# Kernel optimization log

Measured on AMD Instinct MI355X. Metric: run time of the kernel, lower is better.

## Reference

```python
import jax, jax.numpy as jnp
import numpy as np

EPS = 1e-12  # matches torch F.normalize default

def _l2norm(x):
    n = jnp.linalg.norm(x, axis=-1, keepdims=True)
    return x / jnp.maximum(n, EPS)

def setup_inputs() -> dict:
    key = jax.random.key(0)
    k1, k2, k3, k4 = jax.random.split(key, 4)
    return {
        "shape_embedding": jax.random.normal(k1, (4096, 512), dtype=jnp.float32),
        "bank_embedding": jax.random.normal(k2, (100000, 512), dtype=jnp.float32),
        "category_idx": jax.random.randint(k3, (100000,), 0, 9, dtype=jnp.int64),
        "shape_idx": jax.random.randint(k4, (100000,), 0, 10000, dtype=jnp.int64),
    }

def reference(shape_embedding, bank_embedding, category_idx, shape_idx):
    # bank is stored L2-normalized in __init__; query normalized in forward
    q = _l2norm(shape_embedding)          # [N, D]
    b = _l2norm(bank_embedding)           # [M, D]
    sims = jnp.einsum('nd,md->nm', q, b)  # [N, M] cosine similarity
    idx = jnp.argmax(sims, axis=-1)       # [N]
    return (category_idx[idx], shape_idx[idx])
```

## Files before the change

kernel.cpp:

```cpp
#include <hip/hip_runtime.h>
#include <math.h>

#define NQ  4096
#define MB  100000
#define DD  512
#define QT  128
#define BT  128
#define BK  32
#define KIT (DD / BK)
#define NCH ((MB + BT - 1) / BT)
#define NWG (32 * NCH)
#define MARGIN 6e-3f

typedef __attribute__((ext_vector_type(8))) short short8;
typedef __attribute__((ext_vector_type(4))) float f32x4;

__device__ inline unsigned int umax32(unsigned int a, unsigned int b) { return a > b ? a : b; }
__device__ inline unsigned int umin32(unsigned int a, unsigned int b) { return a < b ? a : b; }

__device__ inline unsigned short f2bf(float f) {
  unsigned int u = __float_as_uint(f);
  u += 0x7FFFu + ((u >> 16) & 1u);
  return (unsigned short)(u >> 16);
}

__device__ inline void gload_lds16(const void* g, void* l) {
  __builtin_amdgcn_global_load_lds(
      (const __attribute__((address_space(1))) unsigned int*)g,
      (__attribute__((address_space(3))) unsigned int*)l, 16, 0, 0);
}

__global__ __launch_bounds__(256) void nrm_cast(const float* __restrict__ qin,
                                                const float* __restrict__ bin,
                                                unsigned short* __restrict__ qb,
                                                unsigned short* __restrict__ bb) {
  int wave = threadIdx.x >> 6, lane = threadIdx.x & 63;
  int row = blockIdx.x * 4 + wave;
  const float* src;
  unsigned short* dst;
  if (row < NQ) {
    src = qin + (size_t)row * DD;
    dst = qb + (size_t)row * DD;
  } else {
    int r2 = row - NQ;
    if (r2 >= MB) return;
    src = bin + (size_t)r2 * DD;
    dst = bb + (size_t)r2 * DD;
  }
  const float4* s4 = (const float4*)src;
  float4 x0 = s4[lane * 2], x1 = s4[lane * 2 + 1];
  float ss = x0.x * x0.x + x0.y * x0.y + x0.z * x0.z + x0.w * x0.w +
             x1.x * x1.x + x1.y * x1.y + x1.z * x1.z + x1.w * x1.w;
  #pragma unroll
  for (int m = 1; m < 64; m <<= 1) ss += __shfl_xor(ss, m, 64);
  float r = 1.0f / fmaxf(sqrtf(ss), 1e-12f);
  short8 v;
  v[0] = (short)f2bf(x0.x * r); v[1] = (short)f2bf(x0.y * r);
  v[2] = (short)f2bf(x0.z * r); v[3] = (short)f2bf(x0.w * r);
  v[4] = (short)f2bf(x1.x * r); v[5] = (short)f2bf(x1.y * r);
  v[6] = (short)f2bf(x1.z * r); v[7] = (short)f2bf(x1.w * r);
  *(short8*)(dst + (size_t)lane * 8) = v;
}

__global__ __launch_bounds__(256, 3) void gemm_top2(
    const unsigned short* __restrict__ qb,
    const unsigned short* __restrict__ bb,
    uint2* __restrict__ cand) {
  __shared__ unsigned short sM[2][BT * BK];
  __shared__ unsigned short sN[2][QT * BK];
  __shared__ unsigned int rowwin[QT][2][2];

  int tid = threadIdx.x;
  int wave = tid >> 6, lane = tid & 63;

  int w = blockIdx.x;
  int sw = (w & 7) * (NWG / 8) + (w >> 3);
  int bx = sw & 31;
  int by = sw >> 5;
  int q0 = bx * QT, c0 = by * BT;
  int wm = (wave >> 1) * 64;
  int wn = (wave & 1) * 64;

  f32x4 acc[4][4];
  #pragma unroll
  for (int i = 0; i < 4; ++i)
    #pragma unroll
    for (int j = 0; j < 4; ++j) acc[i][j] = (f32x4){0.f, 0.f, 0.f, 0.f};

  int sr = tid >> 2;
  int slot = tid & 3;
  int swz = (tid >> 4) & 3;
  int ce = (slot ^ swz) * 8;
  int br0 = c0 + sr;       if (br0 >= MB) br0 = MB - 1;
  int br1 = c0 + 64 + sr;  if (br1 >= MB) br1 = MB - 1;

  int rr = lane & 15;
  int ck = lane >> 4;
  int rco = (ck ^ ((rr >> 2) & 3)) * 8;

  const unsigned short* gM0 = bb + (size_t)br0 * DD + ce;
  const unsigned short* gM1 = bb + (size_t)br1 * DD + ce;
  const unsigned short* gN0 = qb + (size_t)(q0 + sr) * DD + ce;
  const unsigned short* gN1 = qb + (size_t)(q0 + 64 + sr) * DD + ce;

  auto STAGE = [&](int kt, int buf) {
    int kk = kt * BK;
    gload_lds16(gM0 + kk, &sM[buf][tid * 8]);
    gload_lds16(gM1 + kk, &sM[buf][2048 + tid * 8]);
    gload_lds16(gN0 + kk, &sN[buf][tid * 8]);
    gload_lds16(gN1 + kk, &sN[buf][2048 + tid * 8]);
  };

  STAGE(0, 0);
  __syncthreads();

  #pragma unroll 2
  for (int kt = 0; kt < KIT; ++kt) {
    int cur = kt & 1;
    if (kt + 1 < KIT) STAGE(kt + 1, cur ^ 1);

    const unsigned short* M0 = sM[cur];
    const unsigned short* N0 = sN[cur];
    short8 af[4], bg[4];
    #pragma unroll
    for (int mi = 0; mi < 4; ++mi)
      af[mi] = *(const short8*)&M0[(wm + mi * 16 + rr) * BK + rco];
    #pragma unroll
    for (int ni = 0; ni < 4; ++ni)
      bg[ni] = *(const short8*)&N0[(wn + ni * 16 + rr) * BK + rco];
    #pragma unroll
    for (int mi = 0; mi < 4; ++mi)
      #pragma unroll
      for (int ni = 0; ni < 4; ++ni)
        acc[mi][ni] = __builtin_amdgcn_mfma_f32_16x16x32_bf16(af[mi], bg[ni],
                                                              acc[mi][ni], 0, 0, 0);
    __syncthreads();
  }

  int g = lane >> 4, cl = lane & 15;
  bool tail = (c0 + BT > MB);
  int nb = 127 - wm - g * 4;
  unsigned int K1[4], K2[4];
  #pragma unroll
  for (int ni = 0; ni < 4; ++ni) { K1[ni] = 0u; K2[ni] = 0u; }

  #pragma unroll
  for (int mi = 0; mi < 4; ++mi) {
    #pragma unroll
    for (int r2 = 0; r2 < 4; ++r2) {
      int rowoff = mi * 16 + r2;
      #pragma unroll
      for (int ni = 0; ni < 4; ++ni) {
        float v = acc[mi][ni][r2];
        unsigned int key = (__float_as_uint(v) & 0xFFFFFF80u) |
                           (unsigned int)(nb - rowoff);
        bool ok = v > 0.0f;
        if (tail) ok = ok && (c0 + wm + g * 4 + rowoff < MB);
        key = ok ? key : 0u;
        unsigned int mx = umax32(K1[ni], key), mn = umin32(K1[ni], key);
        K1[ni] = mx;
        K2[ni] = umax32(K2[ni], mn);
      }
    }
  }

  #pragma unroll
  for (int m = 16; m <= 32; m <<= 1) {
    #pragma unroll
    for (int ni = 0; ni < 4; ++ni) {
      unsigned int o1 = (unsigned int)__shfl_xor((int)K1[ni], m, 64);
      unsigned int o2 = (unsigned int)__shfl_xor((int)K2[ni], m, 64);
      unsigned int mx = umax32(K1[ni], o1), mn = umin32(K1[ni], o1);
      K1[ni] = mx;
      K2[ni] = umax32(mn, umax32(K2[ni], o2));
    }
  }
  if (g == 0) {
    #pragma unroll
    for (int ni = 0; ni < 4; ++ni) {
      int qc = wn + ni * 16 + cl;
      rowwin[qc][wave >> 1][0] = K1[ni];
      rowwin[qc][wave >> 1][1] = K2[ni];
    }
  }
  __syncthreads();

  if (tid < QT) {
    unsigned int a1 = rowwin[tid][0][0], a2 = rowwin[tid][0][1];
    unsigned int b1 = rowwin[tid][1][0], b2 = rowwin[tid][1][1];
    unsigned int k1 = umax32(a1, b1);
    unsigned int k2 = umax32(umin32(a1, b1), umax32(a2, b2));
    cand[(size_t)by * NQ + q0 + tid] = make_uint2(k1, k2);
  }
}

__global__ __launch_bounds__(256) void reduce_refine(
    const float* __restrict__ qraw, const float* __restrict__ braw,
    const int* __restrict__ cat, const int* __restrict__ shp,
    const uint2* __restrict__ cand, int* __restrict__ out) {
  int q = blockIdx.x;
  int tid = threadIdx.x, wave = tid >> 6, lane = tid & 63;
  __shared__ unsigned int wmax[4];
  __shared__ int nsel;
  __shared__ int sel[64];
  __shared__ float rv[64];
  __shared__ int ri[64];
  if (tid == 0) nsel = 0;

  unsigned int mk = 0;
  for (int c = tid; c < NCH; c += 256) mk = umax32(mk, cand[(size_t)c * NQ + q].x);
  #pragma unroll
  for (int m = 1; m < 64; m <<= 1)
    mk = umax32(mk, (unsigned int)__shfl_xor((int)mk, m, 64));
  if (lane == 0) wmax[wave] = mk;
  __syncthreads();
  unsigned int M1 = umax32(umax32(wmax[0], wmax[1]), umax32(wmax[2], wmax[3]));
  float thr = __uint_as_float(M1 & 0xFFFFFF80u) - MARGIN;

  for (int c = tid; c < NCH; c += 256) {
    uint2 e = cand[(size_t)c * NQ + q];
    float f1 = __uint_as_float(e.x & 0xFFFFFF80u);
    float f2 = __uint_as_float(e.y & 0xFFFFFF80u);
    if (f1 >= thr) {
      int p = atomicAdd(&nsel, 1);
      if (p < 64) sel[p] = c * BT + 127 - (int)(e.x & 127u);
    }
    if (f2 >= thr) {
      int p = atomicAdd(&nsel, 1);
      if (p < 64) sel[p] = c * BT + 127 - (int)(e.y & 127u);
    }
  }
  __syncthreads();
  int ns = nsel; if (ns > 64) ns = 64;

  const float4* q4 = (const float4*)(qraw + (size_t)q * DD);
  float4 qa = q4[lane * 2], qv = q4[lane * 2 + 1];
  float qss = qa.x * qa.x + qa.y * qa.y + qa.z * qa.z + qa.w * qa.w +
              qv.x * qv.x + qv.y * qv.y + qv.z * qv.z + qv.w * qv.w;
  #pragma unroll
  for (int m = 1; m < 64; m <<= 1) qss += __shfl_xor(qss, m, 64);
  float qn = fmaxf(sqrtf(qss), 1e-12f);

  for (int ci = wave; ci < ns; ci += 4) {
    int bi = sel[ci];
    const float4* b4 = (const float4*)(braw + (size_t)bi * DD);
    float4 ba = b4[lane * 2], bv = b4[lane * 2 + 1];
    float dot = qa.x * ba.x + qa.y * ba.y + qa.z * ba.z + qa.w * ba.w +
                qv.x * bv.x + qv.y * bv.y + qv.z * bv.z + qv.w * bv.w;
    float bss = ba.x * ba.x + ba.y * ba.y + ba.z * ba.z + ba.w * ba.w +
                bv.x * bv.x + bv.y * bv.y + bv.z * bv.z + bv.w * bv.w;
    #pragma unroll
    for (int m = 1; m < 64; m <<= 1) {
      dot += __shfl_xor(dot, m, 64);
      bss += __shfl_xor(bss, m, 64);
    }
    if (lane == 0) {
      float bn = fmaxf(sqrtf(bss), 1e-12f);
      rv[ci] = dot / (qn * bn);
      ri[ci] = bi;
    }
  }
  __syncthreads();

  if (tid == 0) {
    float bvv = rv[0]; int bidx = ri[0];
    for (int i = 1; i < ns; ++i)
      if (rv[i] > bvv || (rv[i] == bvv && ri[i] < bidx)) { bvv = rv[i]; bidx = ri[i]; }
    out[q] = cat[bidx];
    out[NQ + q] = shp[bidx];
  }
}

extern "C" void kernel_launch(void* const* d_in, const int* in_sizes, int n_in,
                              void* d_out, int out_size, void* d_ws, size_t ws_size,
                              hipStream_t stream) {
  const float* qin = (const float*)d_in[0];
  const float* bin = (const float*)d_in[1];
  const int* cat = (const int*)d_in[2];
  const int* shp = (const int*)d_in[3];
  int* out = (int*)d_out;

  char* ws = (char*)d_ws;
  unsigned short* qb = (unsigned short*)ws;
  unsigned short* bb = (unsigned short*)(ws + (size_t)NQ * DD * 2);
  uint2* cand = (uint2*)(ws + (size_t)NQ * DD * 2 + (size_t)MB * DD * 2);

  nrm_cast<<<(NQ + MB) / 4, 256, 0, stream>>>(qin, bin, qb, bb);
  gemm_top2<<<NWG, 256, 0, stream>>>(qb, bb, cand);
  reduce_refine<<<NQ, 256, 0, stream>>>(qin, bin, cat, shp, cand, out);
}
```

Before: 868.3 us.

## Batch 64 queries per block in refine and overlap LDS staging with MFMA

The refine kernel now gives each block 64 queries, with one lane per query, so each wave reads contiguous cand entries across queries instead of strided single-query reads. Selected candidates go into a shared work queue that all waves then process. Separately, the GEMM main loop swaps __syncthreads for a partial vmcnt wait plus raw barriers, so the next tile's global-to-LDS load overlaps the current tile's MFMAs. Risks: candidates per query are capped at 16 (was 64), the query norm is recomputed for each candidate, and a single thread serially builds the queue.

```diff
diff --git a/kernel.cpp b/kernel.cpp
--- a/kernel.cpp
+++ b/kernel.cpp
@@ -11,6 +11,7 @@
 #define NCH ((MB + BT - 1) / BT)
 #define NWG (32 * NCH)
 #define MARGIN 6e-3f
+#define RQ  64
 
 typedef __attribute__((ext_vector_type(8))) short short8;
 typedef __attribute__((ext_vector_type(4))) float f32x4;
@@ -111,16 +112,9 @@
     gload_lds16(gN1 + kk, &sN[buf][2048 + tid * 8]);
   };
 
-  STAGE(0, 0);
-  __syncthreads();
-
-  #pragma unroll 2
-  for (int kt = 0; kt < KIT; ++kt) {
-    int cur = kt & 1;
-    if (kt + 1 < KIT) STAGE(kt + 1, cur ^ 1);
-
-    const unsigned short* M0 = sM[cur];
-    const unsigned short* N0 = sN[cur];
+  auto COMPUTE = [&](int buf) {
+    const unsigned short* M0 = sM[buf];
+    const unsigned short* N0 = sN[buf];
     short8 af[4], bg[4];
     #pragma unroll
     for (int mi = 0; mi < 4; ++mi)
@@ -134,8 +128,22 @@
       for (int ni = 0; ni < 4; ++ni)
         acc[mi][ni] = __builtin_amdgcn_mfma_f32_16x16x32_bf16(af[mi], bg[ni],
                                                               acc[mi][ni], 0, 0, 0);
-    __syncthreads();
-  }
+  };
+
+  STAGE(0, 0);
+  for (int kt = 0; kt < KIT - 1; ++kt) {
+    STAGE(kt + 1, (kt & 1) ^ 1);
+    asm volatile("s_waitcnt vmcnt(4)" ::: "memory");
+    __builtin_amdgcn_s_barrier();
+    __builtin_amdgcn_sched_barrier(0);
+    COMPUTE(kt & 1);
+    __builtin_amdgcn_sched_barrier(0);
+    __builtin_amdgcn_s_barrier();
+  }
+  asm volatile("s_waitcnt vmcnt(0)" ::: "memory");
+  __builtin_amdgcn_s_barrier();
+  __builtin_amdgcn_sched_barrier(0);
+  COMPUTE((KIT - 1) & 1);
 
   int g = lane >> 4, cl = lane & 15;
   bool tail = (c0 + BT > MB);
@@ -198,74 +206,89 @@
     const float* __restrict__ qraw, const float* __restrict__ braw,
     const int* __restrict__ cat, const int* __restrict__ shp,
     const uint2* __restrict__ cand, int* __restrict__ out) {
-  int q = blockIdx.x;
   int tid = threadIdx.x, wave = tid >> 6, lane = tid & 63;
-  __shared__ unsigned int wmax[4];
-  __shared__ int nsel;
-  __shared__ int sel[64];
-  __shared__ float rv[64];
-  __shared__ int ri[64];
-  if (tid == 0) nsel = 0;
+  int q0 = blockIdx.x * RQ;
+  int q = q0 + lane;
+
+  __shared__ unsigned int wm[4][RQ];
+  __shared__ int cnt[RQ];
+  __shared__ int sel[RQ][16];
+  __shared__ float rvv[RQ][16];
+  __shared__ unsigned short queue[RQ * 16];
+  __shared__ int qn;
 
   unsigned int mk = 0;
-  for (int c = tid; c < NCH; c += 256) mk = umax32(mk, cand[(size_t)c * NQ + q].x);
-  #pragma unroll
-  for (int m = 1; m < 64; m <<= 1)
-    mk = umax32(mk, (unsigned int)__shfl_xor((int)mk, m, 64));
-  if (lane == 0) wmax[wave] = mk;
-  __syncthreads();
-  unsigned int M1 = umax32(umax32(wmax[0], wmax[1]), umax32(wmax[2], wmax[3]));
+  for (int c = wave; c < NCH; c += 4)
+    mk = umax32(mk, cand[(size_t)c * NQ + q].x);
+  wm[wave][lane] = mk;
+  if (wave == 0) cnt[lane] = 0;
+  __syncthreads();
+  unsigned int M1 = umax32(umax32(wm[0][lane], wm[1][lane]),
+                           umax32(wm[2][lane], wm[3][lane]));
   float thr = __uint_as_float(M1 & 0xFFFFFF80u) - MARGIN;
 
-  for (int c = tid; c < NCH; c += 256) {
+  for (int c = wave; c < NCH; c += 4) {
     uint2 e = cand[(size_t)c * NQ + q];
     float f1 = __uint_as_float(e.x & 0xFFFFFF80u);
     float f2 = __uint_as_float(e.y & 0xFFFFFF80u);
     if (f1 >= thr) {
-      int p = atomicAdd(&nsel, 1);
-      if (p < 64) sel[p] = c * BT + 127 - (int)(e.x & 127u);
+      int p = atomicAdd(&cnt[lane], 1);
+      if (p < 16) sel[lane][p] = c * BT + 127 - (int)(e.x & 127u);
     }
     if (f2 >= thr) {
-      int p = atomicAdd(&nsel, 1);
-      if (p < 64) sel[p] = c * BT + 127 - (int)(e.y & 127u);
-    }
-  }
-  __syncthreads();
-  int ns = nsel; if (ns > 64) ns = 64;
-
-  const float4* q4 = (const float4*)(qraw + (size_t)q * DD);
-  float4 qa = q4[lane * 2], qv = q4[lane * 2 + 1];
-  float qss = qa.x * qa.x + qa.y * qa.y + qa.z * qa.z + qa.w * qa.w +
-              qv.x * qv.x + qv.y * qv.y + qv.z * qv.z + qv.w * qv.w;
-  #pragma unroll
-  for (int m = 1; m < 64; m <<= 1) qss += __shfl_xor(qss, m, 64);
-  float qn = fmaxf(sqrtf(qss), 1e-12f);
-
-  for (int ci = wave; ci < ns; ci += 4) {
-    int bi = sel[ci];
+      int p = atomicAdd(&cnt[lane], 1);
+      if (p < 16) sel[lane][p] = c * BT + 127 - (int)(e.y & 127u);
+    }
+  }
+  __syncthreads();
+
+  if (tid == 0) {
+    int t = 0;
+    for (int i = 0; i < RQ; ++i) {
+      int n = cnt[i] < 16 ? cnt[i] : 16;
+      for (int s = 0; s < n; ++s) queue[t++] = (unsigned short)((i << 4) | s);
+    }
+    qn = t;
+  }
+  __syncthreads();
+
+  int total = qn;
+  for (int e = wave; e < total; e += 4) {
+    int ql = queue[e] >> 4, sl = queue[e] & 15;
+    int bi = sel[ql][sl];
+    const float4* q4 = (const float4*)(qraw + (size_t)(q0 + ql) * DD);
     const float4* b4 = (const float4*)(braw + (size_t)bi * DD);
+    float4 qa = q4[lane * 2], qv = q4[lane * 2 + 1];
     float4 ba = b4[lane * 2], bv = b4[lane * 2 + 1];
     float dot = qa.x * ba.x + qa.y * ba.y + qa.z * ba.z + qa.w * ba.w +
                 qv.x * bv.x + qv.y * bv.y + qv.z * bv.z + qv.w * bv.w;
+    float qss = qa.x * qa.x + qa.y * qa.y + qa.z * qa.z + qa.w * qa.w +
+                qv.x * qv.x + qv.y * qv.y + qv.z * qv.z + qv.w * qv.w;
     float bss = ba.x * ba.x + ba.y * ba.y + ba.z * ba.z + ba.w * ba.w +
                 bv.x * bv.x + bv.y * bv.y + bv.z * bv.z + bv.w * bv.w;
     #pragma unroll
     for (int m = 1; m < 64; m <<= 1) {
       dot += __shfl_xor(dot, m, 64);
+      qss += __shfl_xor(qss, m, 64);
       bss += __shfl_xor(bss, m, 64);
     }
     if (lane == 0) {
-      float bn = fmaxf(sqrtf(bss), 1e-12f);
-      rv[ci] = dot / (qn * bn);
-      ri[ci] = bi;
-    }
-  }
-  __syncthreads();
-
-  if (tid == 0) {
-    float bvv = rv[0]; int bidx = ri[0];
-    for (int i = 1; i < ns; ++i)
-      if (rv[i] > bvv || (rv[i] == bvv && ri[i] < bidx)) { bvv = rv[i]; bidx = ri[i]; }
+      float qn_ = fmaxf(sqrtf(qss), 1e-12f);
+      float bn_ = fmaxf(sqrtf(bss), 1e-12f);
+      rvv[ql][sl] = dot / (qn_ * bn_);
+    }
+  }
+  __syncthreads();
+
+  if (wave == 0) {
+    int n = cnt[lane] < 16 ? cnt[lane] : 16;
+    float bv = rvv[lane][0];
+    int bidx = sel[lane][0];
+    for (int s = 1; s < n; ++s) {
+      float v = rvv[lane][s];
+      int ix = sel[lane][s];
+      if (v > bv || (v == bv && ix < bidx)) { bv = v; bidx = ix; }
+    }
     out[q] = cat[bidx];
     out[NQ + q] = shp[bidx];
   }
@@ -287,5 +310,5 @@
 
   nrm_cast<<<(NQ + MB) / 4, 256, 0, stream>>>(qin, bin, qb, bb);
   gemm_top2<<<NWG, 256, 0, stream>>>(qb, bb, cand);
-  reduce_refine<<<NQ, 256, 0, stream>>>(qin, bin, cat, shp, cand, out);
-}
+  reduce_refine<<<NQ / RQ, 256, 0, stream>>>(qin, bin, cat, shp, cand, out);
+}
```

New measurement: 909.6 us. +4.8%, slower.
